# Optimization experiments

Measured on AMD Instinct MI355X. Metric: run time of the kernel, lower is better.

Reference implementation:

```python
import math
import jax, jax.numpy as jnp
import numpy as np

N_HEAD = 16
ROPE_BASE = 10000.0

def setup_inputs() -> dict:
    key = jax.random.key(0)
    k1, k2, k3 = jax.random.split(key, 3)
    B, T, C = 2, 2048, 2048
    x = jax.random.normal(k1, (B, T, C), dtype=jnp.float32)
    Wqkv = jax.random.normal(k2, (C, 3 * C), dtype=jnp.float32) * 0.02  # [C, 3C], y = x @ Wqkv
    Wout = jax.random.normal(k3, (C, C), dtype=jnp.float32) * 0.02
    return {"x": x, "Wqkv": Wqkv, "Wout": Wout}

def _rope_sin_cos(T, half, dtype):
    # build_sin_cos(seq_len, dim=head_size//2): div over arange(0, 2*dim, 2) / (2*dim)
    pos = jnp.arange(T, dtype=jnp.float32)[:, None]                      # [T,1]
    div = jnp.exp(jnp.arange(0, 2 * half, 2, dtype=jnp.float32)
                  * (-math.log(ROPE_BASE) / (2 * half)))                 # [half]
    ang = pos * div                                                      # [T,half]
    return jnp.sin(ang).astype(dtype), jnp.cos(ang).astype(dtype)

def reference(x, Wqkv, Wout):
    B, T, C = x.shape
    H = N_HEAD
    D = C // H
    half = D // 2
    qkv = (x @ Wqkv).reshape(B, T, 3, H, D)
    q, k, v = qkv[:, :, 0], qkv[:, :, 1], qkv[:, :, 2]                   # [B,T,H,D]
    sin, cos = _rope_sin_cos(T, half, x.dtype)
    sin = sin[None, :, None, :]  # [1,T,1,half]
    cos = cos[None, :, None, :]
    def rope(t):
        t1, t2 = t[..., :half], t[..., half:]
        return jnp.concatenate([t1 * cos - t2 * sin, t2 * cos + t1 * sin], axis=-1)
    q, k = rope(q), rope(k)
    scale = 1.0 / math.sqrt(D)  # flash-attn default softmax_scale
    scores = jnp.einsum('bthd,bshd->bhts', q, k) * scale                 # [B,H,T,T]
    causal = jnp.tril(jnp.ones((T, T), dtype=bool))
    scores = jnp.where(causal[None, None], scores, jnp.finfo(scores.dtype).min)
    probs = jax.nn.softmax(scores, axis=-1)
    out = jnp.einsum('bhts,bshd->bhtd', probs, v)                        # [B,H,T,D]
    # Faithful to torch: out.permute(0,2,1,3).reshape(B,T,C) on [B,T,H,D]
    # == flatten of [B,H,T,D] into [B,T,C]
    out = out.reshape(B, T, C)
    return out @ Wout
```

## Files before the change

### kernel.cpp

```cpp
#include <hip/hip_runtime.h>

typedef unsigned short u16;
typedef __attribute__((ext_vector_type(8))) short bf16x8;
typedef __attribute__((ext_vector_type(4))) float f32x4;
typedef __attribute__((ext_vector_type(8))) unsigned short u16x8;

#define B_ 2
#define T_ 2048
#define C_ 2048
#define H_ 16
#define D_ 128
#define QKVW 6144

__device__ __forceinline__ u16 f2b(float f) {
  unsigned int x = __builtin_bit_cast(unsigned int, f);
  x += 0x7fffu + ((x >> 16) & 1u);
  return (u16)(x >> 16);
}
__device__ __forceinline__ float b2f(u16 u) {
  unsigned int x = ((unsigned int)u) << 16;
  return __builtin_bit_cast(float, x);
}
__device__ __forceinline__ void gl_lds16(const void* g, void* l) {
  __builtin_amdgcn_global_load_lds((const __attribute__((address_space(1))) void*)g,
                                   (__attribute__((address_space(3))) void*)l, 16, 0, 0);
}

__global__ void castbf(const float* __restrict__ in, u16* __restrict__ out) {
  int i = blockIdx.x * 256 + threadIdx.x;
  f32x4 a = ((const f32x4*)in)[2 * i];
  f32x4 b = ((const f32x4*)in)[2 * i + 1];
  u16x8 o;
  o[0] = f2b(a[0]); o[1] = f2b(a[1]); o[2] = f2b(a[2]); o[3] = f2b(a[3]);
  o[4] = f2b(b[0]); o[5] = f2b(b[1]); o[6] = f2b(b[2]); o[7] = f2b(b[3]);
  ((u16x8*)out)[i] = o;
}

__global__ __launch_bounds__(256) void castT(const float* __restrict__ in,
                                             u16* __restrict__ out, int K, int N) {
  __shared__ __align__(16) u16 ld[64][72];
  const int nt = blockIdx.x * 64, kt = blockIdx.y * 64;
  const int tid = threadIdx.x;
#pragma unroll
  for (int s = 0; s < 4; ++s) {
    int idx = tid + s * 256;
    int r = idx >> 4;
    int c = (idx & 15) * 4;
    f32x4 v = *(const f32x4*)(in + (size_t)(kt + r) * N + nt + c);
    ld[r][c] = f2b(v[0]); ld[r][c + 1] = f2b(v[1]);
    ld[r][c + 2] = f2b(v[2]); ld[r][c + 3] = f2b(v[3]);
  }
  __syncthreads();
#pragma unroll
  for (int s = 0; s < 2; ++s) {
    int idx = tid + s * 256;
    int n = idx >> 3;
    int c8 = (idx & 7) * 8;
    u16x8 o;
#pragma unroll
    for (int j = 0; j < 8; ++j) o[j] = ld[c8 + j][n];
    *(u16x8*)(out + (size_t)(nt + n) * K + kt + c8) = o;
  }
}

__device__ __forceinline__ void stage_chunk(const u16* __restrict__ g, int K,
                                            u16* l, int ch) {
  int row = ch >> 3;
  int c = (ch & 7) ^ (row & 7);
  gl_lds16(g + (size_t)row * K + c * 8, l + ch * 8);
}

#define MFMA_Q(AF, BF, MH, NH)                                               \
  _Pragma("unroll")                                                          \
  for (int mi = 0; mi < 4; ++mi) {                                           \
    _Pragma("unroll")                                                        \
    for (int ni = 0; ni < 2; ++ni) {                                         \
      _Pragma("unroll")                                                      \
      for (int ks = 0; ks < 2; ++ks)                                         \
        acc[(MH)*4 + mi][(NH)*2 + ni] =                                      \
            __builtin_amdgcn_mfma_f32_16x16x32_bf16(                         \
                AF[mi][ks], BF[ni][ks], acc[(MH)*4 + mi][(NH)*2 + ni],       \
                0, 0, 0);                                                    \
    }                                                                        \
  }

template <int OUT_BF16>
__global__ __launch_bounds__(512, 2) void gemm256(const u16* __restrict__ A,
                                                  const u16* __restrict__ Bt,
                                                  void* __restrict__ Cout,
                                                  int M, int N, int K, int NTILE) {
  __shared__ __align__(16) u16 sm[65536];
  const int tid = threadIdx.x;
  const int lane = tid & 63, w = tid >> 6;
  const int quad = lane >> 4, l15 = lane & 15;
  const int wm = w >> 2, wn = w & 3;
  int id = blockIdx.x;
  const int cpx = gridDim.x >> 3;
  id = (id & 7) * cpx + (id >> 3);
  const int tn0 = (id % NTILE) * 256, tm0 = (id / NTILE) * 256;
  const int NT = K >> 6;
  const u16* Ag = A + (size_t)tm0 * K;
  const u16* Bg = Bt + (size_t)tn0 * K;

  f32x4 acc[8][4] = {};
  bf16x8 a0[4][2], a1[4][2], b0[2][2], b1[2][2];

  auto stA = [&](int tt, int half) {
    u16* l = &sm[(tt & 1) * 32768];
    const u16* g = Ag + tt * 64;
    stage_chunk(g, K, l, half * 512 + tid);
    stage_chunk(g, K, l, 1024 + half * 512 + tid);
  };
  auto stB = [&](int tt, int nh) {
    u16* l = &sm[(tt & 1) * 32768 + 16384];
    const u16* g = Bg + tt * 64;
    int ch = nh * 256 + (tid & 255) + ((tid >> 8) << 9);
    stage_chunk(g, K, l, ch);
    stage_chunk(g, K, l, ch + 1024);
  };

  stA(0, 0); stB(0, 0); stA(0, 1); stB(0, 1);
  if (NT > 1) {
    stA(1, 0); stB(1, 0); stA(1, 1);
    asm volatile("s_waitcnt vmcnt(6)" ::: "memory");
  } else {
    asm volatile("s_waitcnt vmcnt(0)" ::: "memory");
  }
  __builtin_amdgcn_s_barrier();

  for (int t = 0; t < NT; ++t) {
    const u16* LA = &sm[(t & 1) * 32768];
    const u16* LB = LA + 16384;
#pragma unroll
    for (int mi = 0; mi < 4; ++mi)
#pragma unroll
      for (int ks = 0; ks < 2; ++ks) {
        int r = wm * 128 + mi * 16 + l15;
        a0[mi][ks] = *(const bf16x8*)&LA[r * 64 +
                     ((ks * 32 + quad * 8) ^ ((r & 7) << 3))];
      }
#pragma unroll
    for (int ni = 0; ni < 2; ++ni)
#pragma unroll
      for (int ks = 0; ks < 2; ++ks) {
        int r = wn * 64 + ni * 16 + l15;
        b0[ni][ks] = *(const bf16x8*)&LB[r * 64 +
                     ((ks * 32 + quad * 8) ^ ((r & 7) << 3))];
      }
    if (t + 1 < NT) stB(t + 1, 1);
    __builtin_amdgcn_s_barrier();
    asm volatile("s_waitcnt lgkmcnt(0)");
    __builtin_amdgcn_sched_barrier(0);
    __builtin_amdgcn_s_setprio(1);
    MFMA_Q(a0, b0, 0, 0);
    __builtin_amdgcn_s_setprio(0);
    __builtin_amdgcn_s_barrier();
#pragma unroll
    for (int ni = 0; ni < 2; ++ni)
#pragma unroll
      for (int ks = 0; ks < 2; ++ks) {
        int r = wn * 64 + (ni + 2) * 16 + l15;
        b1[ni][ks] = *(const bf16x8*)&LB[r * 64 +
                     ((ks * 32 + quad * 8) ^ ((r & 7) << 3))];
      }
    if (t + 2 < NT) stA(t + 2, 0);
    __builtin_amdgcn_s_barrier();
    asm volatile("s_waitcnt lgkmcnt(0)");
    __builtin_amdgcn_sched_barrier(0);
    __builtin_amdgcn_s_setprio(1);
    MFMA_Q(a0, b1, 0, 1);
    __builtin_amdgcn_s_setprio(0);
    __builtin_amdgcn_s_barrier();
#pragma unroll
    for (int mi = 0; mi < 4; ++mi)
#pragma unroll
      for (int ks = 0; ks < 2; ++ks) {
        int r = wm * 128 + (mi + 4) * 16 + l15;
        a1[mi][ks] = *(const bf16x8*)&LA[r * 64 +
                     ((ks * 32 + quad * 8) ^ ((r & 7) << 3))];
      }
    if (t + 2 < NT) stB(t + 2, 0);
    __builtin_amdgcn_s_barrier();
    asm volatile("s_waitcnt lgkmcnt(0)");
    __builtin_amdgcn_sched_barrier(0);
    __builtin_amdgcn_s_setprio(1);
    MFMA_Q(a1, b1, 1, 1);
    __builtin_amdgcn_s_setprio(0);
    __builtin_amdgcn_s_barrier();
    if (t + 2 < NT) {
      stA(t + 2, 1);
      asm volatile("s_waitcnt vmcnt(6)" ::: "memory");
    } else {
      asm volatile("s_waitcnt vmcnt(0)" ::: "memory");
    }
    __builtin_amdgcn_s_barrier();
    __builtin_amdgcn_s_setprio(1);
    MFMA_Q(a1, b0, 1, 0);
    __builtin_amdgcn_s_setprio(0);
    __builtin_amdgcn_s_barrier();
  }

#pragma unroll
  for (int mi = 0; mi < 8; ++mi)
#pragma unroll
    for (int ni = 0; ni < 4; ++ni)
#pragma unroll
      for (int r = 0; r < 4; ++r) {
        int row = tm0 + wm * 128 + mi * 16 + quad * 4 + r;
        int col = tn0 + wn * 64 + ni * 16 + l15;
        float v = acc[mi][ni][r];
        if (OUT_BF16) ((u16*)Cout)[(size_t)row * N + col] = f2b(v);
        else          ((float*)Cout)[(size_t)row * N + col] = v;
      }
}

template <int OUT_BF16>
__global__ __launch_bounds__(512, 2) void gemmH(const u16* __restrict__ A,
                                                const u16* __restrict__ Bt,
                                                void* __restrict__ Cout,
                                                int M, int N, int K,
                                                int NTILE, int tnbase) {
  __shared__ __align__(16) u16 sm[3][24576];
  const int tid = threadIdx.x;
  const int lane = tid & 63, w = tid >> 6;
  const int quad = lane >> 4, l15 = lane & 15;
  const int wm = w >> 2, wn = w & 3;
  int id = blockIdx.x;
  const int cpx = gridDim.x >> 3;
  id = (id & 7) * cpx + (id >> 3);
  const int tn0 = tnbase + (id % NTILE) * 256, tm0 = (id / NTILE) * 128;
  const int NT = K >> 6;
  const u16* Ag = A + (size_t)tm0 * K;
  const u16* Bg = Bt + (size_t)tn0 * K;

  f32x4 acc[4][4] = {};
  bf16x8 af[4][2], b0[2][2], b1[2][2];

  auto stage6 = [&](int tt) {
    u16* l = sm[tt % 3];
    const u16* g = Ag + tt * 64;
    stage_chunk(g, K, l, tid);
    stage_chunk(g, K, l, 512 + tid);
    const u16* gb = Bg + tt * 64;
#pragma unroll
    for (int h = 0; h < 2; ++h)
#pragma unroll
      for (int s = 0; s < 2; ++s) {
        int ch = s * 512 + tid;
        int ru = ch >> 3, cc = ch & 7;
        int row = ((ru >> 5) << 6) + h * 32 + (ru & 31);
        int csrc = cc ^ (ru & 7);
        gl_lds16(gb + (size_t)row * K + csrc * 8, &l[8192 + h * 8192 + ch * 8]);
      }
  };

  stage6(0);
  if (NT > 1) {
    stage6(1);
    asm volatile("s_waitcnt vmcnt(6)" ::: "memory");
  } else {
    asm volatile("s_waitcnt vmcnt(0)" ::: "memory");
  }
  __builtin_amdgcn_s_barrier();

  for (int t = 0; t < NT; ++t) {
    const u16* L = sm[t % 3];
#pragma unroll
    for (int mi = 0; mi < 4; ++mi)
#pragma unroll
      for (int ks = 0; ks < 2; ++ks) {
        int r = wm * 64 + mi * 16 + l15;
        af[mi][ks] = *(const bf16x8*)&L[r * 64 +
                     ((ks * 32 + quad * 8) ^ ((r & 7) << 3))];
      }
#pragma unroll
    for (int nj = 0; nj < 2; ++nj)
#pragma unroll
      for (int ks = 0; ks < 2; ++ks) {
        int ru = wn * 32 + nj * 16 + l15;
        b0[nj][ks] = *(const bf16x8*)&L[8192 + ru * 64 +
                     ((ks * 32 + quad * 8) ^ ((ru & 7) << 3))];
      }
    if (t + 2 < NT) stage6(t + 2);
    __builtin_amdgcn_s_barrier();
    asm volatile("s_waitcnt lgkmcnt(0)");
    __builtin_amdgcn_sched_barrier(0);
    __builtin_amdgcn_s_setprio(1);
#pragma unroll
    for (int mi = 0; mi < 4; ++mi)
#pragma unroll
      for (int nj = 0; nj < 2; ++nj)
#pragma unroll
        for (int ks = 0; ks < 2; ++ks)
          acc[mi][nj] = __builtin_amdgcn_mfma_f32_16x16x32_bf16(af[mi][ks], b0[nj][ks], acc[mi][nj], 0, 0, 0);
    __builtin_amdgcn_s_setprio(0);
    __builtin_amdgcn_s_barrier();
#pragma unroll
    for (int nj = 0; nj < 2; ++nj)
#pragma unroll
      for (int ks = 0; ks < 2; ++ks) {
        int ru = wn * 32 + nj * 16 + l15;
        b1[nj][ks] = *(const bf16x8*)&L[16384 + ru * 64 +
                     ((ks * 32 + quad * 8) ^ ((ru & 7) << 3))];
      }
    if (t + 2 < NT)
      asm volatile("s_waitcnt vmcnt(6)" ::: "memory");
    else
      asm volatile("s_waitcnt vmcnt(0)" ::: "memory");
    __builtin_amdgcn_s_barrier();
    asm volatile("s_waitcnt lgkmcnt(0)");
    __builtin_amdgcn_sched_barrier(0);
    __builtin_amdgcn_s_setprio(1);
#pragma unroll
    for (int mi = 0; mi < 4; ++mi)
#pragma unroll
      for (int nj = 0; nj < 2; ++nj)
#pragma unroll
        for (int ks = 0; ks < 2; ++ks)
          acc[mi][nj + 2] = __builtin_amdgcn_mfma_f32_16x16x32_bf16(af[mi][ks], b1[nj][ks], acc[mi][nj + 2], 0, 0, 0);
    __builtin_amdgcn_s_setprio(0);
    __builtin_amdgcn_s_barrier();
  }

#pragma unroll
  for (int mi = 0; mi < 4; ++mi)
#pragma unroll
    for (int nj = 0; nj < 4; ++nj)
#pragma unroll
      for (int r = 0; r < 4; ++r) {
        int row = tm0 + wm * 64 + mi * 16 + quad * 4 + r;
        int col = tn0 + wn * 64 + nj * 16 + l15;
        float v = acc[mi][nj][r];
        if (OUT_BF16) ((u16*)Cout)[(size_t)row * N + col] = f2b(v);
        else          ((float*)Cout)[(size_t)row * N + col] = v;
      }
}

__global__ void rope_k(u16* __restrict__ qkv) {
  int g = blockIdx.x * 256 + threadIdx.x;
  int i0 = (g & 7) * 8;
  int h = (g >> 3) & 15;
  int which = (g >> 7) & 1;
  int t = (g >> 8) & 2047;
  int b = g >> 19;
  size_t base = (size_t)(b * T_ + t) * QKVW + which * 2048 + h * 128 + i0;
  const float qs = which ? 1.0f : 0.08838834764831845f * 1.4426950408889634f;
  u16x8 v1 = *(const u16x8*)(qkv + base);
  u16x8 v2 = *(const u16x8*)(qkv + base + 64);
  u16x8 o1, o2;
#pragma unroll
  for (int j = 0; j < 8; ++j) {
    int i = i0 + j;
    float t1 = b2f(v1[j]), t2 = b2f(v2[j]);
    float ang = (float)t * exp2f(-(float)i * 0.20762050593046439f);
    float sn, cs;
    sincosf(ang, &sn, &cs);
    o1[j] = f2b((t1 * cs - t2 * sn) * qs);
    o2[j] = f2b((t2 * cs + t1 * sn) * qs);
  }
  *(u16x8*)(qkv + base) = o1;
  *(u16x8*)(qkv + base + 64) = o2;
}

__global__ __launch_bounds__(256) void vtrans(const u16* __restrict__ qkv, u16* __restrict__ vt) {
  __shared__ __align__(16) u16 ld[128][136];
  const int tt = blockIdx.x, bh = blockIdx.y;
  const int b = bh >> 4, h = bh & 15;
  const u16* vb = qkv + (size_t)b * T_ * QKVW + 4096 + h * 128;
  const int tid = threadIdx.x;
#pragma unroll
  for (int s = 0; s < 8; ++s) {
    int t = (tid >> 4) + s * 16;
    int d0 = (tid & 15) * 8;
    *(bf16x8*)&ld[t][d0] = *(const bf16x8*)(vb + (size_t)(tt * 128 + t) * QKVW + d0);
  }
  __syncthreads();
  u16* vout = vt + (size_t)bh * D_ * T_ + tt * 128;
#pragma unroll
  for (int s = 0; s < 8; ++s) {
    int d = (tid >> 4) + s * 16;
    int t0 = (tid & 15) * 8;
    u16x8 o;
#pragma unroll
    for (int j = 0; j < 8; ++j) o[j] = ld[t0 + j][d];
    *(u16x8*)(vout + (size_t)d * T_ + t0) = o;
  }
}

#define APW 76
__global__ __launch_bounds__(256, 2) void attn(const u16* __restrict__ qkv,
                                               const u16* __restrict__ vt,
                                               u16* __restrict__ obuf) {
  __shared__ __align__(16) u16 lK[2][64 * 128];
  __shared__ __align__(16) u16 lV[2][128 * 64];
  __shared__ __align__(16) u16 lP[64 * APW];
  const int tid = threadIdx.x, lane = tid & 63, w = tid >> 6;
  const int quad = lane >> 4, l15 = lane & 15;
  const int bh = blockIdx.x, jp = blockIdx.y;
  const int jA = jp, jB = 31 - jp;
  const int b = bh >> 4, h = bh & 15;
  const u16* qb = qkv + (size_t)b * T_ * QKVW + h * 128;
  const u16* kb = qb + 2048;
  const u16* vtb = vt + (size_t)bh * D_ * T_;

  bf16x8 qfA[4], qfB[4];
#pragma unroll
  for (int kk = 0; kk < 4; ++kk) {
    qfA[kk] = *(const bf16x8*)(qb + (size_t)(jA * 64 + w * 16 + l15) * QKVW + kk * 32 + quad * 8);
    qfB[kk] = *(const bf16x8*)(qb + (size_t)(jB * 64 + w * 16 + l15) * QKVW + kk * 32 + quad * 8);
  }

  f32x4 oA[8] = {}, oB[8] = {};
  float mA[4], lAr[4], mB[4], lBr[4];
#pragma unroll
  for (int r = 0; r < 4; ++r) {
    mA[r] = -__builtin_inff(); lAr[r] = 0.f;
    mB[r] = -__builtin_inff(); lBr[r] = 0.f;
  }

  auto stage = [&](int kt, int buf) {
#pragma unroll
    for (int s = 0; s < 4; ++s) {
      int ch = tid + s * 256;
      int kr = ch >> 4, kc = (ch & 15) ^ (kr & 7);
      gl_lds16(kb + (size_t)(kt * 64 + kr) * QKVW + kc * 8, &lK[buf][ch * 8]);
      int vr = ch >> 3, vc = (ch & 7) ^ (vr & 7);
      gl_lds16(vtb + (size_t)vr * T_ + kt * 64 + vc * 8, &lV[buf][ch * 8]);
    }
  };

  auto smpv = [&](f32x4* sacc, f32x4* oacc, float* mrow, float* lrow,
                  int jw, int kt, int cb) {
    if (kt == jw) {
#pragma unroll
      for (int nj = 0; nj < 4; ++nj) {
        int key = nj * 16 + l15;
#pragma unroll
        for (int r = 0; r < 4; ++r) {
          int qrow = w * 16 + quad * 4 + r;
          if (key > qrow) sacc[nj][r] = -__builtin_inff();
        }
      }
    }
    float pm[4];
#pragma unroll
    for (int r = 0; r < 4; ++r)
      pm[r] = fmaxf(fmaxf(sacc[0][r], sacc[1][r]), fmaxf(sacc[2][r], sacc[3][r]));
    float dmax = fmaxf(fmaxf(pm[0] - mrow[0], pm[1] - mrow[1]),
                       fmaxf(pm[2] - mrow[2], pm[3] - mrow[3]));
    if (__any(dmax > 11.5f)) {
#pragma unroll
      for (int r = 0; r < 4; ++r) {
        float rm = pm[r];
        rm = fmaxf(rm, __shfl_xor(rm, 1));
        rm = fmaxf(rm, __shfl_xor(rm, 2));
        rm = fmaxf(rm, __shfl_xor(rm, 4));
        rm = fmaxf(rm, __shfl_xor(rm, 8));
        float mold = mrow[r];
        float mnew = fmaxf(mold, rm);
        float alpha = exp2f(mold - mnew);
#pragma unroll
        for (int nd = 0; nd < 8; ++nd) oacc[nd][r] *= alpha;
        lrow[r] *= alpha;
        mrow[r] = mnew;
      }
    }
#pragma unroll
    for (int r = 0; r < 4; ++r) {
      int prow = w * 16 + quad * 4 + r;
      float rs = 0.f;
#pragma unroll
      for (int nj = 0; nj < 4; ++nj) {
        float p = exp2f(sacc[nj][r] - mrow[r]);
        rs += p;
        lP[prow * APW + nj * 16 + l15] = f2b(p);
      }
      lrow[r] += rs;
    }
#pragma unroll
    for (int kk = 0; kk < 2; ++kk) {
      bf16x8 pf, vf[8];
      pf = *(const bf16x8*)&lP[(w * 16 + l15) * APW + kk * 32 + quad * 8];
#pragma unroll
      for (int nd = 0; nd < 8; ++nd) {
        int r = nd * 16 + l15;
        vf[nd] = *(const bf16x8*)&lV[cb][r * 64 + ((kk * 32 + quad * 8) ^ ((r & 7) << 3))];
      }
      __builtin_amdgcn_s_setprio(1);
#pragma unroll
      for (int nd = 0; nd < 8; ++nd)
        oacc[nd] = __builtin_amdgcn_mfma_f32_16x16x32_bf16(pf, vf[nd], oacc[nd], 0, 0, 0);
      __builtin_amdgcn_s_setprio(0);
    }
  };

  stage(0, 0);
  __syncthreads();

  for (int kt = 0; kt <= jB; ++kt) {
    int cb = kt & 1;
    if (kt < jB) stage(kt + 1, cb ^ 1);
    const bool doA = (kt <= jA);
    f32x4 sB[4] = {}, sA[4] = {};
#pragma unroll
    for (int kk = 0; kk < 4; ++kk) {
      bf16x8 kf[4];
#pragma unroll
      for (int nj = 0; nj < 4; ++nj) {
        int r = nj * 16 + l15;
        kf[nj] = *(const bf16x8*)&lK[cb][r * 128 + ((kk * 32 + quad * 8) ^ ((r & 7) << 3))];
      }
      __builtin_amdgcn_s_setprio(1);
#pragma unroll
      for (int nj = 0; nj < 4; ++nj)
        sB[nj] = __builtin_amdgcn_mfma_f32_16x16x32_bf16(qfB[kk], kf[nj], sB[nj], 0, 0, 0);
      if (doA)
#pragma unroll
        for (int nj = 0; nj < 4; ++nj)
          sA[nj] = __builtin_amdgcn_mfma_f32_16x16x32_bf16(qfA[kk], kf[nj], sA[nj], 0, 0, 0);
      __builtin_amdgcn_s_setprio(0);
    }
    smpv(sB, oB, mB, lBr, jB, kt, cb);
    if (doA) smpv(sA, oA, mA, lAr, jA, kt, cb);
    __syncthreads();
  }

#pragma unroll
  for (int r = 0; r < 4; ++r) {
    float sA = lAr[r], sB = lBr[r];
    sA += __shfl_xor(sA, 1); sB += __shfl_xor(sB, 1);
    sA += __shfl_xor(sA, 2); sB += __shfl_xor(sB, 2);
    sA += __shfl_xor(sA, 4); sB += __shfl_xor(sB, 4);
    sA += __shfl_xor(sA, 8); sB += __shfl_xor(sB, 8);
    lAr[r] = sA; lBr[r] = sB;
  }

#pragma unroll
  for (int nd = 0; nd < 8; ++nd)
#pragma unroll
    for (int r = 0; r < 4; ++r) {
      int dcol = nd * 16 + l15;
      int qrB = jB * 64 + w * 16 + quad * 4 + r;
      obuf[((size_t)bh * T_ + qrB) * D_ + dcol] = f2b(oB[nd][r] / lBr[r]);
      int qrA = jA * 64 + w * 16 + quad * 4 + r;
      obuf[((size_t)bh * T_ + qrA) * D_ + dcol] = f2b(oA[nd][r] / lAr[r]);
    }
}

extern "C" void kernel_launch(void* const* d_in, const int* in_sizes, int n_in,
                              void* d_out, int out_size, void* d_ws, size_t ws_size,
                              hipStream_t stream) {
  const float* x = (const float*)d_in[0];
  const float* Wqkv = (const float*)d_in[1];
  const float* Wout = (const float*)d_in[2];
  float* out = (float*)d_out;
  char* ws = (char*)d_ws;

  u16* xb   = (u16*)ws;
  u16* wqt  = (u16*)(ws + 16777216);
  u16* qkvb = (u16*)(ws + 41943040);
  u16* vtb  = (u16*)(ws + 92274688);
  u16* wot  = wqt;
  u16* ob   = xb;

  castbf<<<4096, 256, 0, stream>>>(x, xb);
  castT<<<dim3(96, 32), 256, 0, stream>>>(Wqkv, wqt, 2048, 6144);
  gemm256<1><<<dim3(256), 512, 0, stream>>>(xb, wqt, qkvb, 4096, 6144, 2048, 16);
  gemmH<1><<<dim3(256), 512, 0, stream>>>(xb, wqt, qkvb, 4096, 6144, 2048, 8, 4096);
  castT<<<dim3(32, 32), 256, 0, stream>>>(Wout, wot, 2048, 2048);
  rope_k<<<4096, 256, 0, stream>>>(qkvb);
  vtrans<<<dim3(16, 32), 256, 0, stream>>>(qkvb, vtb);
  attn<<<dim3(32, 16), 256, 0, stream>>>(qkvb, vtb, ob);
  gemmH<0><<<dim3(256), 512, 0, stream>>>(ob, wot, out, 4096, 2048, 2048, 8, 0);
}
```

Measured before the change: 369.7 us.

## Single-buffer K/V LDS in attention to fit three blocks per CU

Replaces the double-buffered K and V LDS tiles with single buffers and raises launch bounds to 3 blocks per CU. The next K tile is now loaded after the QK^T phase and the next V tile after the PV phase, with extra barriers between them. The aim is higher occupancy from the smaller LDS footprint. In exchange, the global-to-LDS load for each tile is only partly overlapped with compute, each iteration carries two more barriers, and the tighter launch bound may squeeze registers.

```diff
diff --git a/kernel.cpp b/kernel.cpp
--- a/kernel.cpp
+++ b/kernel.cpp
@@ -388,11 +388,11 @@
 }
 
 #define APW 76
-__global__ __launch_bounds__(256, 2) void attn(const u16* __restrict__ qkv,
+__global__ __launch_bounds__(256, 3) void attn(const u16* __restrict__ qkv,
                                                const u16* __restrict__ vt,
                                                u16* __restrict__ obuf) {
-  __shared__ __align__(16) u16 lK[2][64 * 128];
-  __shared__ __align__(16) u16 lV[2][128 * 64];
+  __shared__ __align__(16) u16 lK[64 * 128];
+  __shared__ __align__(16) u16 lV[128 * 64];
   __shared__ __align__(16) u16 lP[64 * APW];
   const int tid = threadIdx.x, lane = tid & 63, w = tid >> 6;
   const int quad = lane >> 4, l15 = lane & 15;
@@ -418,19 +418,25 @@
     mB[r] = -__builtin_inff(); lBr[r] = 0.f;
   }
 
-  auto stage = [&](int kt, int buf) {
+  auto stageK = [&](int kt) {
 #pragma unroll
     for (int s = 0; s < 4; ++s) {
       int ch = tid + s * 256;
       int kr = ch >> 4, kc = (ch & 15) ^ (kr & 7);
-      gl_lds16(kb + (size_t)(kt * 64 + kr) * QKVW + kc * 8, &lK[buf][ch * 8]);
+      gl_lds16(kb + (size_t)(kt * 64 + kr) * QKVW + kc * 8, &lK[ch * 8]);
+    }
+  };
+  auto stageV = [&](int kt) {
+#pragma unroll
+    for (int s = 0; s < 4; ++s) {
+      int ch = tid + s * 256;
       int vr = ch >> 3, vc = (ch & 7) ^ (vr & 7);
-      gl_lds16(vtb + (size_t)vr * T_ + kt * 64 + vc * 8, &lV[buf][ch * 8]);
+      gl_lds16(vtb + (size_t)vr * T_ + kt * 64 + vc * 8, &lV[ch * 8]);
     }
   };
 
   auto smpv = [&](f32x4* sacc, f32x4* oacc, float* mrow, float* lrow,
-                  int jw, int kt, int cb) {
+                  int jw, int kt) {
     if (kt == jw) {
 #pragma unroll
       for (int nj = 0; nj < 4; ++nj) {
@@ -484,7 +490,7 @@
 #pragma unroll
       for (int nd = 0; nd < 8; ++nd) {
         int r = nd * 16 + l15;
-        vf[nd] = *(const bf16x8*)&lV[cb][r * 64 + ((kk * 32 + quad * 8) ^ ((r & 7) << 3))];
+        vf[nd] = *(const bf16x8*)&lV[r * 64 + ((kk * 32 + quad * 8) ^ ((r & 7) << 3))];
       }
       __builtin_amdgcn_s_setprio(1);
 #pragma unroll
@@ -494,12 +500,10 @@
     }
   };
 
-  stage(0, 0);
+  stageK(0); stageV(0);
   __syncthreads();
 
   for (int kt = 0; kt <= jB; ++kt) {
-    int cb = kt & 1;
-    if (kt < jB) stage(kt + 1, cb ^ 1);
     const bool doA = (kt <= jA);
     f32x4 sB[4] = {}, sA[4] = {};
 #pragma unroll
@@ -508,7 +512,7 @@
 #pragma unroll
       for (int nj = 0; nj < 4; ++nj) {
         int r = nj * 16 + l15;
-        kf[nj] = *(const bf16x8*)&lK[cb][r * 128 + ((kk * 32 + quad * 8) ^ ((r & 7) << 3))];
+        kf[nj] = *(const bf16x8*)&lK[r * 128 + ((kk * 32 + quad * 8) ^ ((r & 7) << 3))];
       }
       __builtin_amdgcn_s_setprio(1);
 #pragma unroll
@@ -520,8 +524,12 @@
           sA[nj] = __builtin_amdgcn_mfma_f32_16x16x32_bf16(qfA[kk], kf[nj], sA[nj], 0, 0, 0);
       __builtin_amdgcn_s_setprio(0);
     }
-    smpv(sB, oB, mB, lBr, jB, kt, cb);
-    if (doA) smpv(sA, oA, mA, lAr, jA, kt, cb);
+    __syncthreads();
+    if (kt < jB) stageK(kt + 1);
+    smpv(sB, oB, mB, lBr, jB, kt);
+    if (doA) smpv(sA, oA, mA, lAr, jA, kt);
+    __syncthreads();
+    if (kt < jB) stageV(kt + 1);
     __syncthreads();
   }
 
```

After: 473.3 us. 1.28x slower.
